# Performance work log

Measured on AMD Instinct MI355X. Metric: run time of the kernel, lower is better.

## Reference

```python
import jax, jax.numpy as jnp
import numpy as np

N_NODES = 100_000
N_EDGES = 800_000
N_RELS = 2
NEG_SLOPE = 0.2  # DGL GATConv default negative_slope


def _gat_conv(x, src, dst, W, al, ar, b, n_nodes):
    """One DGL-style GATConv over one relation's edge list.
    x: (N, F_in); src/dst: (E,); W: (F_in, H*D); al/ar: (H, D); b: (H*D,).
    Returns (N, H, D). Zero in-degree nodes get just the bias (softmax empty)."""
    H, D = al.shape
    feat = (x @ W).reshape(-1, H, D)                      # (N, H, D)
    el = jnp.sum(feat * al, axis=-1)                      # (N, H)
    er = jnp.sum(feat * ar, axis=-1)                      # (N, H)
    e = jax.nn.leaky_relu(el[src] + er[dst], NEG_SLOPE)   # (E, H) edge scores
    # segment softmax over incoming edges of each dst node
    m = jax.ops.segment_max(e, dst, num_segments=n_nodes)  # (N, H)
    m = jax.lax.stop_gradient(jnp.where(jnp.isfinite(m), m, 0.0))
    ex = jnp.exp(e - m[dst])                              # (E, H)
    s = jax.ops.segment_sum(ex, dst, num_segments=n_nodes)  # (N, H)
    alpha = ex / s[dst]                                   # (E, H); s[dst] > 0 on edges
    # weighted scatter-aggregate of source features
    out = jax.ops.segment_sum(alpha[:, :, None] * feat[src], dst,
                              num_segments=n_nodes)       # (N, H, D)
    return out + b.reshape(H, D)


def reference(x, W1, al1, ar1, b1, W2, al2, ar2, b2, src, dst):
    n = x.shape[0]
    n_rels = src.shape[0]
    # layer 1: per-relation GATConv (2 heads), mean across relations
    h1 = sum(_gat_conv(x, src[r], dst[r], W1[r], al1[r], ar1[r], b1[r], n)
             for r in range(n_rels)) / n_rels             # (N, 2, 64)
    h1 = jax.nn.relu(h1.reshape(n, -1))                   # flatten(1) + relu -> (N, 128)
    # layer 2: per-relation GATConv (1 head), mean across relations, squeeze head
    h2 = sum(_gat_conv(h1, src[r], dst[r], W2[r], al2[r], ar2[r], b2[r], n)
             for r in range(n_rels)) / n_rels             # (N, 1, 128)
    return h2[:, 0, :]                                    # (N, 128)


def setup_inputs() -> dict:
    key = jax.random.key(0)
    ks = jax.random.split(key, 11)
    f = lambda k, s: jax.random.normal(k, s, dtype=jnp.float32) * 0.1
    return {
        "x": jax.random.normal(ks[0], (N_NODES, 128), dtype=jnp.float32),
        "W1": f(ks[1], (N_RELS, 128, 128)),
        "al1": f(ks[2], (N_RELS, 2, 64)),
        "ar1": f(ks[3], (N_RELS, 2, 64)),
        "b1": jnp.zeros((N_RELS, 128), jnp.float32),
        "W2": f(ks[4], (N_RELS, 128, 128)),
        "al2": f(ks[5], (N_RELS, 1, 128)),
        "ar2": f(ks[6], (N_RELS, 1, 128)),
        "b2": jnp.zeros((N_RELS, 128), jnp.float32),
        "src": jax.random.randint(ks[7], (N_RELS, N_EDGES), 0, N_NODES, dtype=jnp.int32),
        "dst": jax.random.randint(ks[8], (N_RELS, N_EDGES), 0, N_NODES, dtype=jnp.int32),
    }
```

## Files before the change

kernel.cpp:

```cpp
#include <hip/hip_runtime.h>
#include <hip/hip_bf16.h>
#include <math.h>

#define NN 100000
#define NE 800000
#define FD 128

#define BKW 512
#define NBK 391
#define CAP 4608
#define CHUNK 8192

typedef unsigned short ushort_t;
typedef __attribute__((ext_vector_type(8))) short bf16x8;
typedef __attribute__((ext_vector_type(4))) float f32x4;

union U8 { uint4 u; bf16x8 b; };

__device__ inline unsigned f2bf(float f){
    unsigned u = __float_as_uint(f);
    return (u + 0x7fffu + ((u >> 16) & 1u)) >> 16;
}
__device__ inline unsigned cvtpk(float lo, float hi){
    unsigned r;
    asm("v_cvt_pk_bf16_f32 %0, %1, %2" : "=v"(r) : "v"(lo), "v"(hi));
    return r;
}
__device__ inline float blo(unsigned p){ return __uint_as_float(p << 16); }
__device__ inline float bhi(unsigned p){ return __uint_as_float(p & 0xffff0000u); }
__device__ inline float2 up2(unsigned p){ float2 f; f.x = blo(p); f.y = bhi(p); return f; }
__device__ inline void pkfma(float2& d, float2 a, float2 b){
    asm("v_pk_fma_f32 %0, %1, %2, %0" : "+v"(d) : "v"(a), "v"(b));
}

__global__ void k_binit(int* __restrict__ bcur){
    int t = blockIdx.x * blockDim.x + threadIdx.x;
    if (t < NBK) bcur[t] = t * CAP;
}

__global__ __launch_bounds__(256) void k_part(const int* __restrict__ dst,
                                              const int* __restrict__ src,
                                              int* __restrict__ bcur,
                                              uint2* __restrict__ ebuf){
    __shared__ int lcount[NBK];
    __shared__ int lbase[NBK];
    int t = threadIdx.x;
    long base = (long)blockIdx.x * CHUNK;
    for (int j = t; j < NBK; j += 256) lcount[j] = 0;
    __syncthreads();
    #pragma unroll 4
    for (int k = 0; k < CHUNK/256; k++){
        long i = base + k*256 + t;
        if (i < 2*NE){
            int b = (dst[i] + ((i >= NE) ? NN : 0)) >> 9;
            atomicAdd(&lcount[b], 1);
        }
    }
    __syncthreads();
    for (int j = t; j < NBK; j += 256){
        int c = lcount[j];
        lbase[j] = c ? atomicAdd(&bcur[j], c) : 0;
    }
    __syncthreads();
    for (int j = t; j < NBK; j += 256) lcount[j] = 0;
    __syncthreads();
    #pragma unroll 4
    for (int k = 0; k < CHUNK/256; k++){
        long i = base + k*256 + t;
        if (i < 2*NE){
            int dstU = dst[i] + ((i >= NE) ? NN : 0);
            int b = dstU >> 9;
            int r = atomicAdd(&lcount[b], 1);
            int pos = lbase[b] + r;
            if (pos < (b + 1) * CAP)
                ebuf[pos] = make_uint2((unsigned)src[i], (unsigned)dstU);
        }
    }
}

__global__ __launch_bounds__(512) void k_bktscan(const int* __restrict__ bcur,
                                                 int* __restrict__ gbase,
                                                 int* __restrict__ rowptr){
    __shared__ int sm[512];
    int t = threadIdx.x;
    int v = (t < NBK) ? min(bcur[t] - t*CAP, CAP) : 0;
    sm[t] = v; __syncthreads();
    for (int off = 1; off < 512; off <<= 1){
        int add = (t >= off) ? sm[t-off] : 0;
        __syncthreads();
        sm[t] += add;
        __syncthreads();
    }
    if (t <= NBK) gbase[t] = sm[t] - v;
    if (t == 0) rowptr[2*NN] = 2*NE;
}

__global__ __launch_bounds__(256) void k_bscatter(const uint2* __restrict__ ebuf,
                                                  const int* __restrict__ bcur,
                                                  const int* __restrict__ gbase,
                                                  int* __restrict__ rowptr,
                                                  int* __restrict__ colsrc){
    __shared__ int lhist[BKW];
    __shared__ int lcur[BKW];
    __shared__ int sm[256];
    int b = blockIdx.x;
    int n0 = b * BKW;
    int nloc = min(2*NN, n0 + BKW) - n0;
    int ecnt = min(bcur[b] - b*CAP, CAP);
    const uint2* eb = ebuf + (size_t)b * CAP;
    int t = threadIdx.x;
    lhist[2*t] = 0; lhist[2*t+1] = 0;
    __syncthreads();
    for (int i = t; i < ecnt; i += 256)
        atomicAdd(&lhist[eb[i].y - n0], 1);
    __syncthreads();
    int a0 = lhist[2*t], a1 = lhist[2*t+1];
    int ps = a0 + a1;
    sm[t] = ps; __syncthreads();
    for (int off = 1; off < 256; off <<= 1){
        int add = (t >= off) ? sm[t-off] : 0;
        __syncthreads();
        sm[t] += add;
        __syncthreads();
    }
    int excl = sm[t] - ps;
    int g = gbase[b];
    int p0 = g + excl, p1 = g + excl + a0;
    if (2*t     < nloc) rowptr[n0 + 2*t]     = p0;
    if (2*t + 1 < nloc) rowptr[n0 + 2*t + 1] = p1;
    lcur[2*t] = p0; lcur[2*t+1] = p1;
    __syncthreads();
    for (int i = t; i < ecnt; i += 256){
        uint2 e = eb[i];
        int p = atomicAdd(&lcur[e.y - n0], 1);
        colsrc[p] = (int)e.x;
    }
}

__global__ void k_prepw2(const float* __restrict__ W1, const float* __restrict__ W2,
                         ushort_t* __restrict__ Wt1, ushort_t* __restrict__ Wt2){
    int idx = blockIdx.x * blockDim.x + threadIdx.x;
    if (idx >= 65536) return;
    int m = idx >> 15;
    int i = idx & 32767;
    const float* W = m ? W2 : W1;
    ushort_t* Wt   = m ? Wt2 : Wt1;
    int j  = i & 7;
    int l  = (i >> 3) & 63;
    int ks = (i >> 9) & 3;
    int f  = i >> 11;
    int k  = ks*32 + (l >> 4)*8 + j;
    if (m) k = (((k & 7) >> 1) + 4*(k & 1))*16 + (k >> 3);
    int col = (f & 7)*16 + (l & 15);
    int rel = f >> 3;
    Wt[i] = (ushort_t)f2bf(W[rel*16384 + k*FD + col]);
}

__device__ inline float red16(float v){
    v += __shfl_xor(v, 1);
    v += __shfl_xor(v, 2);
    v += __shfl_xor(v, 4);
    v += __shfl_xor(v, 8);
    return v;
}

template<int H, bool AF32>
__global__ __launch_bounds__(256) void k_gemm_mfma(
        const ushort_t* __restrict__ Ab, const float* __restrict__ Af,
        const ushort_t* __restrict__ Wt,
        const float* __restrict__ al0, const float* __restrict__ ar0,
        const float* __restrict__ al1, const float* __restrict__ ar1,
        ushort_t* __restrict__ featb0, ushort_t* __restrict__ featb1,
        float* __restrict__ el0, float* __restrict__ er0,
        float* __restrict__ el1, float* __restrict__ er1){
    int t = threadIdx.x;
    int w = t >> 6, l = t & 63;
    int c = l & 15, kgrp = l >> 4;
    const bf16x8* WtV = (const bf16x8*)Wt;
    long arow = (long)blockIdx.x*64 + w*16 + c;
    bf16x8 zero8 = {0,0,0,0,0,0,0,0};
    bf16x8 af[4];
    bool rok = arow < NN;
    if (AF32){
        const float4* xv = (const float4*)Af;
        #pragma unroll
        for (int ks = 0; ks < 4; ks++){
            if (rok){
                float4 u = xv[arow*32 + (ks*4 + kgrp)*2];
                float4 v = xv[arow*32 + (ks*4 + kgrp)*2 + 1];
                U8 q;
                q.u = make_uint4(cvtpk(u.x,u.y), cvtpk(u.z,u.w),
                                 cvtpk(v.x,v.y), cvtpk(v.z,v.w));
                af[ks] = q.b;
            } else af[ks] = zero8;
        }
    } else {
        const bf16x8* AbV = (const bf16x8*)Ab;
        #pragma unroll
        for (int ks = 0; ks < 4; ks++)
            af[ks] = rok ? AbV[arow*16 + ks*4 + kgrp] : zero8;
    }
    f32x4 acc[16];
    #pragma unroll
    for (int f = 0; f < 16; f++) acc[f] = (f32x4){0.f,0.f,0.f,0.f};
    #pragma unroll
    for (int f = 0; f < 16; f++){
        #pragma unroll
        for (int ks = 0; ks < 4; ks++){
            acc[f] = __builtin_amdgcn_mfma_f32_16x16x32_bf16(
                         af[ks], WtV[(f*4 + ks)*64 + l], acc[f], 0, 0, 0);
        }
    }
    float alv0[8], arv0[8], alv1[8], arv1[8];
    #pragma unroll
    for (int f = 0; f < 8; f++){
        alv0[f] = al0[f*16 + c]; arv0[f] = ar0[f*16 + c];
        alv1[f] = al1[f*16 + c]; arv1[f] = ar1[f*16 + c];
    }
    #pragma unroll
    for (int reg = 0; reg < 4; reg++){
        long orow = (long)blockIdx.x*64 + w*16 + kgrp*4 + reg;
        bool ok = orow < NN;
        if (ok){
            uint4 p0, p1;
            p0.x = cvtpk(acc[0][reg],  acc[4][reg]);
            p0.y = cvtpk(acc[1][reg],  acc[5][reg]);
            p0.z = cvtpk(acc[2][reg],  acc[6][reg]);
            p0.w = cvtpk(acc[3][reg],  acc[7][reg]);
            p1.x = cvtpk(acc[8][reg],  acc[12][reg]);
            p1.y = cvtpk(acc[9][reg],  acc[13][reg]);
            p1.z = cvtpk(acc[10][reg], acc[14][reg]);
            p1.w = cvtpk(acc[11][reg], acc[15][reg]);
            *(uint4*)&featb0[orow*FD + c*8] = p0;
            *(uint4*)&featb1[orow*FD + c*8] = p1;
        }
        if (H == 2){
            float pl00=0, pr00=0, pl01=0, pr01=0;
            float pl10=0, pr10=0, pl11=0, pr11=0;
            #pragma unroll
            for (int f = 0; f < 4; f++){
                pl00 = fmaf(acc[f][reg],    alv0[f],   pl00);
                pr00 = fmaf(acc[f][reg],    arv0[f],   pr00);
                pl01 = fmaf(acc[4+f][reg],  alv0[4+f], pl01);
                pr01 = fmaf(acc[4+f][reg],  arv0[4+f], pr01);
                pl10 = fmaf(acc[8+f][reg],  alv1[f],   pl10);
                pr10 = fmaf(acc[8+f][reg],  arv1[f],   pr10);
                pl11 = fmaf(acc[12+f][reg], alv1[4+f], pl11);
                pr11 = fmaf(acc[12+f][reg], arv1[4+f], pr11);
            }
            pl00 = red16(pl00); pr00 = red16(pr00);
            pl01 = red16(pl01); pr01 = red16(pr01);
            pl10 = red16(pl10); pr10 = red16(pr10);
            pl11 = red16(pl11); pr11 = red16(pr11);
            if (c == 0 && ok){
                el0[orow*2] = pl00; el0[orow*2+1] = pl01;
                er0[orow*2] = pr00; er0[orow*2+1] = pr01;
                el1[orow*2] = pl10; el1[orow*2+1] = pl11;
                er1[orow*2] = pr10; er1[orow*2+1] = pr11;
            }
        } else {
            float pl0=0, pr0=0, pl1=0, pr1=0;
            #pragma unroll
            for (int f = 0; f < 8; f++){
                pl0 = fmaf(acc[f][reg],   alv0[f], pl0);
                pr0 = fmaf(acc[f][reg],   arv0[f], pr0);
                pl1 = fmaf(acc[8+f][reg], alv1[f], pl1);
                pr1 = fmaf(acc[8+f][reg], arv1[f], pr1);
            }
            pl0 = red16(pl0); pr0 = red16(pr0);
            pl1 = red16(pl1); pr1 = red16(pr1);
            if (c == 0 && ok){
                el0[orow] = pl0; er0[orow] = pr0;
                el1[orow] = pl1; er1[orow] = pr1;
            }
        }
    }
}

template<int H>
__global__ __launch_bounds__(256) void k_agg2(
                       const int* __restrict__ rowptr,
                       const int* __restrict__ colsrc,
                       const float* __restrict__ el0, const float* __restrict__ er0,
                       const float* __restrict__ el1, const float* __restrict__ er1,
                       const ushort_t* __restrict__ featb0, const ushort_t* __restrict__ featb1,
                       const float* __restrict__ bias0, const float* __restrict__ bias1,
                       ushort_t* __restrict__ outb, float* __restrict__ outf){
    int lane = threadIdx.x & 63;
    int half = lane >> 5;
    int hl   = lane & 31;
    int sub  = lane & 15;
    int g    = (lane >> 4) & 1;
    int node = ((blockIdx.x * blockDim.x + threadIdx.x) >> 6) * 2 + half;
    if (node >= NN) return;
    int base0 = rowptr[node],       end0 = rowptr[node+1];
    int base1 = rowptr[NN + node],  end1 = rowptr[NN + node + 1];
    bool has0 = end0 > base0, has1 = end1 > base1;
    float er00 = er0[node*H];
    float er01 = (H == 2) ? er0[node*H + 1] : 0.f;
    float er10 = er1[node*H];
    float er11 = (H == 2) ? er1[node*H + 1] : 0.f;
    float2 ap0[4], ap1[4];
    #pragma unroll
    for (int i = 0; i < 4; i++){ ap0[i] = make_float2(0.f,0.f); ap1[i] = make_float2(0.f,0.f); }
    float s00=0.f, s01=0.f, s10=0.f, s11=0.f;
    while (base0 < end0 || base1 < end1){
        int nrem0 = end0 - base0, nrem1 = end1 - base1;
        bool act0 = hl < nrem0, act1 = hl < nrem1;
        int sv0 = act0 ? colsrc[base0 + hl] : 0;
        int sv1 = act1 ? colsrc[base1 + hl] : 0;
        float a00=0.f, a01=0.f, a10=0.f, a11=0.f;
        if (act0){
            if (H == 2){
                float2 e2 = *(const float2*)&el0[sv0*2];
                float e0 = e2.x + er00, e1 = e2.y + er01;
                e0 = (e0 > 0.f) ? e0 : 0.2f*e0;
                e1 = (e1 > 0.f) ? e1 : 0.2f*e1;
                a00 = __expf(e0); a01 = __expf(e1);
            } else {
                float e0 = el0[sv0] + er00;
                e0 = (e0 > 0.f) ? e0 : 0.2f*e0;
                a00 = __expf(e0);
            }
        }
        if (act1){
            if (H == 2){
                float2 e2 = *(const float2*)&el1[sv1*2];
                float e0 = e2.x + er10, e1 = e2.y + er11;
                e0 = (e0 > 0.f) ? e0 : 0.2f*e0;
                e1 = (e1 > 0.f) ? e1 : 0.2f*e1;
                a10 = __expf(e0); a11 = __expf(e1);
            } else {
                float e0 = el1[sv1] + er10;
                e0 = (e0 > 0.f) ? e0 : 0.2f*e0;
                a10 = __expf(e0);
            }
        }
        s00 += a00; s01 += a01; s10 += a10; s11 += a11;
        int nn0 = (nrem0 > 0) ? min(32, nrem0) : 0;
        int nn1 = (nrem1 > 0) ? min(32, nrem1) : 0;
        int nnm = (nn0 > nn1) ? nn0 : nn1;
        for (int j4 = 0; j4 < nnm; j4 += 4){
            int slA = (half << 5) + j4 + g;
            int slB = slA + 2;
            int sj0A = __shfl(sv0, slA), sj0B = __shfl(sv0, slB);
            int sj1A = __shfl(sv1, slA), sj1B = __shfl(sv1, slB);
            float2 w0A, w0B, w1A, w1B;
            w0A.x = __shfl(a00, slA); w0A.y = (H == 2) ? __shfl(a01, slA) : w0A.x;
            w0B.x = __shfl(a00, slB); w0B.y = (H == 2) ? __shfl(a01, slB) : w0B.x;
            w1A.x = __shfl(a10, slA); w1A.y = (H == 2) ? __shfl(a11, slA) : w1A.x;
            w1B.x = __shfl(a10, slB); w1B.y = (H == 2) ? __shfl(a11, slB) : w1B.x;
            uint4 p0A = *(const uint4*)&featb0[(unsigned)sj0A*FD + sub*8];
            uint4 p0B = *(const uint4*)&featb0[(unsigned)sj0B*FD + sub*8];
            uint4 p1A = *(const uint4*)&featb1[(unsigned)sj1A*FD + sub*8];
            uint4 p1B = *(const uint4*)&featb1[(unsigned)sj1B*FD + sub*8];
            pkfma(ap0[0], w0A, up2(p0A.x));
            pkfma(ap0[1], w0A, up2(p0A.y));
            pkfma(ap0[2], w0A, up2(p0A.z));
            pkfma(ap0[3], w0A, up2(p0A.w));
            pkfma(ap0[0], w0B, up2(p0B.x));
            pkfma(ap0[1], w0B, up2(p0B.y));
            pkfma(ap0[2], w0B, up2(p0B.z));
            pkfma(ap0[3], w0B, up2(p0B.w));
            pkfma(ap1[0], w1A, up2(p1A.x));
            pkfma(ap1[1], w1A, up2(p1A.y));
            pkfma(ap1[2], w1A, up2(p1A.z));
            pkfma(ap1[3], w1A, up2(p1A.w));
            pkfma(ap1[0], w1B, up2(p1B.x));
            pkfma(ap1[1], w1B, up2(p1B.y));
            pkfma(ap1[2], w1B, up2(p1B.z));
            pkfma(ap1[3], w1B, up2(p1B.w));
        }
        base0 += 32; base1 += 32;
    }
    #pragma unroll
    for (int off = 16; off > 0; off >>= 1){
        s00 += __shfl_xor(s00, off);
        s10 += __shfl_xor(s10, off);
        if (H == 2){ s01 += __shfl_xor(s01, off); s11 += __shfl_xor(s11, off); }
    }
    #pragma unroll
    for (int i = 0; i < 4; i++){
        ap0[i].x += __shfl_xor(ap0[i].x, 16); ap0[i].y += __shfl_xor(ap0[i].y, 16);
        ap1[i].x += __shfl_xor(ap1[i].x, 16); ap1[i].y += __shfl_xor(ap1[i].y, 16);
    }
    if (hl < 16){
        float i00 = has0 ? 1.f/s00 : 0.f;
        float i01 = (H == 2) ? (has0 ? 1.f/s01 : 0.f) : i00;
        float i10 = has1 ? 1.f/s10 : 0.f;
        float i11 = (H == 2) ? (has1 ? 1.f/s11 : 0.f) : i10;
        float2 vp[4];
        #pragma unroll
        for (int t = 0; t < 4; t++){
            float bx = bias0[t*16 + sub]       + bias1[t*16 + sub];
            float by = bias0[(t+4)*16 + sub]   + bias1[(t+4)*16 + sub];
            vp[t].x = 0.5f*(ap0[t].x*i00 + ap1[t].x*i10 + bx);
            vp[t].y = 0.5f*(ap0[t].y*i01 + ap1[t].y*i11 + by);
        }
        if (H == 2){
            #pragma unroll
            for (int t = 0; t < 4; t++){
                vp[t].x = fmaxf(vp[t].x, 0.f);
                vp[t].y = fmaxf(vp[t].y, 0.f);
            }
            uint4 o;
            o.x = cvtpk(vp[0].x, vp[0].y); o.y = cvtpk(vp[1].x, vp[1].y);
            o.z = cvtpk(vp[2].x, vp[2].y); o.w = cvtpk(vp[3].x, vp[3].y);
            *(uint4*)&outb[(size_t)node*FD + sub*8] = o;
        } else {
            #pragma unroll
            for (int t = 0; t < 4; t++){
                outf[(size_t)node*FD + t*16 + sub]     = vp[t].x;
                outf[(size_t)node*FD + (t+4)*16 + sub] = vp[t].y;
            }
        }
    }
}

extern "C" void kernel_launch(void* const* d_in, const int* in_sizes, int n_in,
                              void* d_out, int out_size, void* d_ws, size_t ws_size,
                              hipStream_t stream){
    const float* x   = (const float*)d_in[0];
    const float* W1  = (const float*)d_in[1];
    const float* al1 = (const float*)d_in[2];
    const float* ar1 = (const float*)d_in[3];
    const float* b1  = (const float*)d_in[4];
    const float* W2  = (const float*)d_in[5];
    const float* al2 = (const float*)d_in[6];
    const float* ar2 = (const float*)d_in[7];
    const float* b2  = (const float*)d_in[8];
    const int*   src = (const int*)d_in[9];
    const int*   dst = (const int*)d_in[10];
    float* out = (float*)d_out;

    size_t off = 0;
    auto carve = [&](size_t bytes) -> char* {
        char* p = (char*)d_ws + off;
        off += (bytes + 255) & ~(size_t)255;
        return p;
    };
    ushort_t* h1b    = (ushort_t*)carve((size_t)NN * FD * 2);
    ushort_t* featb0 = (ushort_t*)carve((size_t)NN * FD * 2);
    ushort_t* featb1 = (ushort_t*)carve((size_t)NN * FD * 2);
    ushort_t* Wt1    = (ushort_t*)carve(32768 * 2);
    ushort_t* Wt2    = (ushort_t*)carve(32768 * 2);
    float* el0      = (float*)carve((size_t)NN * 2 * 4);
    float* er0      = (float*)carve((size_t)NN * 2 * 4);
    float* el1      = (float*)carve((size_t)NN * 2 * 4);
    float* er1      = (float*)carve((size_t)NN * 2 * 4);
    int*   rowptrA  = (int*)  carve((size_t)(2*NN + 1) * 4);
    int*   colsrcA  = (int*)  carve((size_t)2*NE * 4);
    int*   bcur     = (int*)  carve((size_t)NBK * 4);
    int*   gbase    = (int*)  carve((size_t)(NBK + 1) * 4);
    if (off > ws_size) return;
    uint2* ebuf = (uint2*)featb0;

    const int PB = (2*NE + CHUNK - 1) / CHUNK;
    const int GB = (NN + 63) / 64;
    const int WB = (NN + 7) / 8;

    k_prepw2<<<256, 256, 0, stream>>>(W1, W2, Wt1, Wt2);

    k_binit<<<2, 256, 0, stream>>>(bcur);
    k_part<<<PB, 256, 0, stream>>>(dst, src, bcur, ebuf);
    k_bktscan<<<1, 512, 0, stream>>>(bcur, gbase, rowptrA);
    k_bscatter<<<NBK, 256, 0, stream>>>(ebuf, bcur, gbase, rowptrA, colsrcA);

    k_gemm_mfma<2, true><<<GB, 256, 0, stream>>>(nullptr, x, Wt1,
                                           al1, ar1, al1 + FD, ar1 + FD,
                                           featb0, featb1, el0, er0, el1, er1);
    k_agg2<2><<<WB, 256, 0, stream>>>(rowptrA, colsrcA,
                                      el0, er0, el1, er1, featb0, featb1,
                                      b1, b1 + FD, h1b, nullptr);

    k_gemm_mfma<1, false><<<GB, 256, 0, stream>>>(h1b, nullptr, Wt2,
                                           al2, ar2, al2 + FD, ar2 + FD,
                                           featb0, featb1, el0, er0, el1, er1);
    k_agg2<1><<<WB, 256, 0, stream>>>(rowptrA, colsrcA,
                                      el0, er0, el1, er1, featb0, featb1,
                                      b2, b2 + FD, nullptr, out);
}
```

Baseline: 288.4 us.

## Stage edge data in LDS, replace shuffles with LDS broadcast, fold bucket init

The aggregation kernel now writes each lane's source index and attention weights into a per-wave shared-memory staging buffer and reads them back as float4, replacing many __shfl cross-lane ops per inner step. The bucket scatter kernel caches its edge bucket in shared memory (36 KB) so the second pass reads LDS instead of re-reading global memory. The bucket-cursor init kernel is merged into the weight-prep kernel to save one launch. The added LDS use can lower occupancy in the scatter kernel, and the staging relies on in-wave ordering without explicit barriers.

```diff
diff --git a/kernel.cpp b/kernel.cpp
--- a/kernel.cpp
+++ b/kernel.cpp
@@ -31,11 +31,6 @@
 __device__ inline float2 up2(unsigned p){ float2 f; f.x = blo(p); f.y = bhi(p); return f; }
 __device__ inline void pkfma(float2& d, float2 a, float2 b){
     asm("v_pk_fma_f32 %0, %1, %2, %0" : "+v"(d) : "v"(a), "v"(b));
-}
-
-__global__ void k_binit(int* __restrict__ bcur){
-    int t = blockIdx.x * blockDim.x + threadIdx.x;
-    if (t < NBK) bcur[t] = t * CAP;
 }
 
 __global__ __launch_bounds__(256) void k_part(const int* __restrict__ dst,
@@ -100,6 +95,7 @@
                                                   const int* __restrict__ gbase,
                                                   int* __restrict__ rowptr,
                                                   int* __restrict__ colsrc){
+    __shared__ uint2 se[CAP];
     __shared__ int lhist[BKW];
     __shared__ int lcur[BKW];
     __shared__ int sm[256];
@@ -111,8 +107,11 @@
     int t = threadIdx.x;
     lhist[2*t] = 0; lhist[2*t+1] = 0;
     __syncthreads();
-    for (int i = t; i < ecnt; i += 256)
-        atomicAdd(&lhist[eb[i].y - n0], 1);
+    for (int i = t; i < ecnt; i += 256){
+        uint2 e = eb[i];
+        se[i] = e;
+        atomicAdd(&lhist[e.y - n0], 1);
+    }
     __syncthreads();
     int a0 = lhist[2*t], a1 = lhist[2*t+1];
     int ps = a0 + a1;
@@ -131,16 +130,21 @@
     lcur[2*t] = p0; lcur[2*t+1] = p1;
     __syncthreads();
     for (int i = t; i < ecnt; i += 256){
-        uint2 e = eb[i];
+        uint2 e = se[i];
         int p = atomicAdd(&lcur[e.y - n0], 1);
         colsrc[p] = (int)e.x;
     }
 }
 
 __global__ void k_prepw2(const float* __restrict__ W1, const float* __restrict__ W2,
-                         ushort_t* __restrict__ Wt1, ushort_t* __restrict__ Wt2){
+                         ushort_t* __restrict__ Wt1, ushort_t* __restrict__ Wt2,
+                         int* __restrict__ bcur){
     int idx = blockIdx.x * blockDim.x + threadIdx.x;
-    if (idx >= 65536) return;
+    if (idx >= 65536){
+        int t = idx - 65536;
+        if (t < NBK) bcur[t] = t * CAP;
+        return;
+    }
     int m = idx >> 15;
     int i = idx & 32767;
     const float* W = m ? W2 : W1;
@@ -286,6 +290,8 @@
                        const ushort_t* __restrict__ featb0, const ushort_t* __restrict__ featb1,
                        const float* __restrict__ bias0, const float* __restrict__ bias1,
                        ushort_t* __restrict__ outb, float* __restrict__ outf){
+    __shared__ float4 stg[4][2][2][32];
+    int wid  = threadIdx.x >> 6;
     int lane = threadIdx.x & 63;
     int half = lane >> 5;
     int hl   = lane & 31;
@@ -337,23 +343,28 @@
             }
         }
         s00 += a00; s01 += a01; s10 += a10; s11 += a11;
+        stg[wid][half][0][hl] = make_float4(__int_as_float(sv0), a00,
+                                            (H == 2) ? a01 : a00, 0.f);
+        stg[wid][half][1][hl] = make_float4(__int_as_float(sv1), a10,
+                                            (H == 2) ? a11 : a10, 0.f);
+        __builtin_amdgcn_sched_barrier(0);
         int nn0 = (nrem0 > 0) ? min(32, nrem0) : 0;
         int nn1 = (nrem1 > 0) ? min(32, nrem1) : 0;
         int nnm = (nn0 > nn1) ? nn0 : nn1;
         for (int j4 = 0; j4 < nnm; j4 += 4){
-            int slA = (half << 5) + j4 + g;
-            int slB = slA + 2;
-            int sj0A = __shfl(sv0, slA), sj0B = __shfl(sv0, slB);
-            int sj1A = __shfl(sv1, slA), sj1B = __shfl(sv1, slB);
-            float2 w0A, w0B, w1A, w1B;
-            w0A.x = __shfl(a00, slA); w0A.y = (H == 2) ? __shfl(a01, slA) : w0A.x;
-            w0B.x = __shfl(a00, slB); w0B.y = (H == 2) ? __shfl(a01, slB) : w0B.x;
-            w1A.x = __shfl(a10, slA); w1A.y = (H == 2) ? __shfl(a11, slA) : w1A.x;
-            w1B.x = __shfl(a10, slB); w1B.y = (H == 2) ? __shfl(a11, slB) : w1B.x;
-            uint4 p0A = *(const uint4*)&featb0[(unsigned)sj0A*FD + sub*8];
-            uint4 p0B = *(const uint4*)&featb0[(unsigned)sj0B*FD + sub*8];
-            uint4 p1A = *(const uint4*)&featb1[(unsigned)sj1A*FD + sub*8];
-            uint4 p1B = *(const uint4*)&featb1[(unsigned)sj1B*FD + sub*8];
+            int sA = j4 + g, sB = sA + 2;
+            float4 e0A = stg[wid][half][0][sA];
+            float4 e0B = stg[wid][half][0][sB];
+            float4 e1A = stg[wid][half][1][sA];
+            float4 e1B = stg[wid][half][1][sB];
+            uint4 p0A = *(const uint4*)&featb0[__float_as_uint(e0A.x)*FD + sub*8];
+            uint4 p0B = *(const uint4*)&featb0[__float_as_uint(e0B.x)*FD + sub*8];
+            uint4 p1A = *(const uint4*)&featb1[__float_as_uint(e1A.x)*FD + sub*8];
+            uint4 p1B = *(const uint4*)&featb1[__float_as_uint(e1B.x)*FD + sub*8];
+            float2 w0A = make_float2(e0A.y, e0A.z);
+            float2 w0B = make_float2(e0B.y, e0B.z);
+            float2 w1A = make_float2(e1A.y, e1A.z);
+            float2 w1B = make_float2(e1B.y, e1B.z);
             pkfma(ap0[0], w0A, up2(p0A.x));
             pkfma(ap0[1], w0A, up2(p0A.y));
             pkfma(ap0[2], w0A, up2(p0A.z));
@@ -458,10 +469,10 @@
     const int PB = (2*NE + CHUNK - 1) / CHUNK;
     const int GB = (NN + 63) / 64;
     const int WB = (NN + 7) / 8;
-
-    k_prepw2<<<256, 256, 0, stream>>>(W1, W2, Wt1, Wt2);
-
-    k_binit<<<2, 256, 0, stream>>>(bcur);
+    const int PWB = (65536 + NBK + 255) / 256;
+
+    k_prepw2<<<PWB, 256, 0, stream>>>(W1, W2, Wt1, Wt2, bcur);
+
     k_part<<<PB, 256, 0, stream>>>(dst, src, bcur, ebuf);
     k_bktscan<<<1, 512, 0, stream>>>(bcur, gbase, rowptrA);
     k_bscatter<<<NBK, 256, 0, stream>>>(ebuf, bcur, gbase, rowptrA, colsrcA);
```

Result: no change. 283.9 us (-1.6%).
